# Optimization experiments

Measured on AMD Instinct MI355X. Metric: run time of the kernel, lower is better.

The kernel has to match this reference:

```python
import jax, jax.numpy as jnp
import numpy as np

B, N, K = 32, 64, 128          # batch, atoms per cell, channel width (128x0e + 128x1o)
R_MAX = 5.0
NUM_BESSEL = 8
P_CUT = 5                       # num_polynomial_cutoff
AVG_NEIGH = 16.0                # avg_num_neighbors
H_MLP = 512                     # hidden_dimensions_size, n_hidden_dimensions = 2
FEAT = 5 * K                    # ((num_interactions-1)*4 + 1) * 128 = 640


def silu(x):
    return x * jax.nn.sigmoid(x)


def _bessel_cutoff(r, mask):
    # Bessel radial basis * polynomial cutoff (MACE), masked on valid edges.
    n = jnp.arange(1, NUM_BESSEL + 1, dtype=r.dtype)
    rb = jnp.sqrt(2.0 / R_MAX) * jnp.sin(n * (jnp.pi / R_MAX) * r[..., None]) / r[..., None]
    u = r / R_MAX
    p = float(P_CUT)
    fc = 1.0 - 0.5 * (p + 1) * (p + 2) * u**P_CUT + p * (p + 2) * u**(P_CUT + 1) - 0.5 * p * (p + 1) * u**(P_CUT + 2)
    fc = fc * (u < 1.0)
    return rb * (fc * mask)[..., None]


def _sph(uvec):
    # Real spherical harmonics l=0,1,2 (component normalization), uvec: unit edge vectors.
    x, y, z = uvec[..., 0], uvec[..., 1], uvec[..., 2]
    s3, s5, s15 = 3.0**0.5, 5.0**0.5, 15.0**0.5
    Y0 = jnp.ones_like(x)[..., None]
    Y1 = jnp.stack([s3 * x, s3 * y, s3 * z], -1)
    Y2 = jnp.stack([s15 * x * y, s15 * y * z, 0.5 * s5 * (3 * z * z - 1.0),
                    s15 * x * z, 0.5 * s15 * (x * x - y * y)], -1)
    return Y0, Y1, Y2


def _radial_mlp(x, w0, b0, w1, b1, w2, b2, w3, b3):
    h = silu(x @ w0 + b0)
    h = silu(h @ w1 + b1)
    h = silu(h @ w2 + b2)
    return h @ w3 + b3


def setup_inputs() -> dict:
    key = jax.random.key(0)
    ks = jax.random.split(key, 32)
    f32 = jnp.float32

    def lin(k, fan_in, shape):
        return (jax.random.normal(k, shape, dtype=f32) / np.sqrt(fan_in)).astype(f32)

    inp = {
        "noisy_relative_positions": jax.random.uniform(ks[0], (B, N, 3), dtype=f32),
        "time": jax.random.uniform(ks[1], (B, 1), dtype=f32),
        "unit_cell": (11.0 * jnp.eye(3, dtype=f32) + 0.3 * jax.random.uniform(ks[2], (B, 3, 3), dtype=f32)),
        "w_embed": lin(ks[3], 1, (K,)),
        # interaction 1 radial MLP: 8 -> 64 -> 64 -> 64 -> 3*K (weights for l=0,1,2 paths)
        "r1_w0": lin(ks[4], NUM_BESSEL, (NUM_BESSEL, 64)), "r1_b0": jnp.zeros((64,), f32),
        "r1_w1": lin(ks[5], 64, (64, 64)), "r1_b1": jnp.zeros((64,), f32),
        "r1_w2": lin(ks[6], 64, (64, 64)), "r1_b2": jnp.zeros((64,), f32),
        "r1_w3": lin(ks[7], 64, (64, 3 * K)), "r1_b3": jnp.zeros((3 * K,), f32),
        "mix1_l0": lin(ks[8], K, (K, K)),
        "mix1_l1": lin(ks[9], K, (K, K)),
        "mix1_l2": lin(ks[10], K, (K, K)),
        # interaction 2 radial MLP: 8 -> 64 -> 64 -> 64 -> 2*K (paths 0e x 0e -> 0e, 1o x 1o -> 0e)
        "r2_w0": lin(ks[11], NUM_BESSEL, (NUM_BESSEL, 64)), "r2_b0": jnp.zeros((64,), f32),
        "r2_w1": lin(ks[12], 64, (64, 64)), "r2_b1": jnp.zeros((64,), f32),
        "r2_w2": lin(ks[13], 64, (64, 64)), "r2_b2": jnp.zeros((64,), f32),
        "r2_w3": lin(ks[14], 64, (64, 2 * K)), "r2_b3": jnp.zeros((2 * K,), f32),
        "mix2": lin(ks[15], K, (K, K)),
        # readout MLP: 641 -> 512 -> 512 -> 3
        "mlp_w0": lin(ks[16], FEAT + 1, (FEAT + 1, H_MLP)), "mlp_b0": jnp.zeros((H_MLP,), f32),
        "mlp_w1": lin(ks[17], H_MLP, (H_MLP, H_MLP)), "mlp_b1": jnp.zeros((H_MLP,), f32),
        "mlp_w2": lin(ks[18], H_MLP, (H_MLP, 3)), "mlp_b2": jnp.zeros((3,), f32),
    }
    return inp


def reference(noisy_relative_positions, time, unit_cell, w_embed,
              r1_w0, r1_b0, r1_w1, r1_b1, r1_w2, r1_b2, r1_w3, r1_b3,
              mix1_l0, mix1_l1, mix1_l2,
              r2_w0, r2_b0, r2_w1, r2_b1, r2_w2, r2_b2, r2_w3, r2_b3, mix2,
              mlp_w0, mlp_b0, mlp_w1, mlp_b1, mlp_w2, mlp_b2):
    frac = noisy_relative_positions                      # [B,N,3] fractional
    d = frac[:, :, None, :] - frac[:, None, :, :]        # [B,N,N,3]
    d = d - jnp.round(d)                                 # minimum-image PBC
    dc = jnp.einsum('bijc,bcd->bijd', d, unit_cell)      # cartesian displacements
    r = jnp.sqrt(jnp.maximum(jnp.sum(dc * dc, -1), 1e-12))
    mask = (r < R_MAX) & (~jnp.eye(N, dtype=bool))[None]
    r_safe = jnp.where(mask, r, 1.0)
    uvec = dc / r_safe[..., None] * mask[..., None]      # unit edge vectors (0 off-edge)

    rad = _bessel_cutoff(r_safe, mask)                   # [B,N,N,8]
    Y0, Y1, Y2 = _sph(uvec)                              # [B,N,N,1|3|5]

    h0 = jnp.broadcast_to(w_embed, (B, N, K))            # element embedding (single species)

    # ---- interaction 1: radial-weighted tensor product h_j (x) Y_l, scatter over j ----
    we = _radial_mlp(rad, r1_w0, r1_b0, r1_w1, r1_b1, r1_w2, r1_b2, r1_w3, r1_b3)
    we = we.reshape(B, N, N, 3, K) * mask[..., None, None]
    hj = h0[:, None, :, :]                               # sender features [B,1,N,K]
    msg0 = jnp.einsum('bijk,bijm->bimk', we[..., 0, :] * hj, Y0)[:, :, 0] / AVG_NEIGH  # [B,N,K]
    msg1 = jnp.einsum('bijk,bijm->bimk', we[..., 1, :] * hj, Y1) / AVG_NEIGH           # [B,N,3,K]
    msg2 = jnp.einsum('bijk,bijm->bimk', we[..., 2, :] * hj, Y2) / AVG_NEIGH           # [B,N,5,K]

    s1 = msg0 @ mix1_l0 + jnp.sum(msg2 * msg2, axis=2) @ mix1_l2   # scalars [B,N,K]
    v1 = jnp.einsum('bimk,kc->bimc', msg1, mix1_l1)                # vectors [B,N,3,K]
    h1 = silu(s1)

    # ---- interaction 2: scalar output from 0e x 0e and 1o x 1o -> 0e paths ----
    we2 = _radial_mlp(rad, r2_w0, r2_b0, r2_w1, r2_b1, r2_w2, r2_b2, r2_w3, r2_b3)
    we2 = we2.reshape(B, N, N, 2, K) * mask[..., None, None]
    msg_a = jnp.sum(we2[..., 0, :] * h1[:, None, :, :], axis=2)    # [B,N,K]
    inv = jnp.einsum('bijm,bjmk->bijk', Y1, v1)                    # Y1 . v1_j invariant
    msg_b = jnp.sum(we2[..., 1, :] * inv, axis=2)
    s2 = ((msg_a + msg_b) / AVG_NEIGH) @ mix2                      # [B,N,K]

    # node_feats: layer1 full irreps (128x0e + 128x1o -> 512) + layer2 scalars (128) = 640
    node_feats = jnp.concatenate([s1, v1.reshape(B, N, 3 * K), s2], axis=-1)

    t = jnp.broadcast_to(time[:, None, :], (B, N, 1))
    x = jnp.concatenate([node_feats, t], axis=-1)                  # [B,N,641]
    x = jax.nn.relu(x @ mlp_w0 + mlp_b0)
    x = jax.nn.relu(x @ mlp_w1 + mlp_b1)
    return x @ mlp_w2 + mlp_b2                                     # [B,N,3]
```

## Files before the change

kernel.cpp:

```cpp
#include <hip/hip_runtime.h>
#include <math.h>

#define B_ 32
#define N_ 64
#define K_ 128
#define NPAIR (B_*N_*N_)
#define NTRI 2080
#define GEOM_BLOCKS 260
#define PREP_COUNT 741376
#define PREP_BLOCKS 2896

typedef __attribute__((ext_vector_type(8))) short short8;
typedef __attribute__((ext_vector_type(8))) __bf16 bf16x8;
typedef __attribute__((ext_vector_type(4))) float floatx4;

__device__ __forceinline__ float silu_f(float x) {
    float e = __builtin_amdgcn_exp2f(-1.442695040888963f * x);
    return x * __builtin_amdgcn_rcpf(1.0f + e);
}
__device__ __forceinline__ float4 ld4(const float* p) { return *(const float4*)p; }

__device__ __forceinline__ short f2bf(float x) {
    union { float f; unsigned u; } v; v.f = x;
    unsigned r = (v.u + 0x7FFFu + ((v.u >> 16) & 1u)) >> 16;
    return (short)r;
}
__device__ __forceinline__ float bf2f(short s) {
    union { unsigned u; float f; } v;
    v.u = ((unsigned)(unsigned short)s) << 16;
    return v.f;
}
__device__ __forceinline__ bf16x8 ld_frag(const short* p) {
    short8 r = *(const short8*)p;
    return __builtin_bit_cast(bf16x8, r);
}

__device__ __forceinline__ int2 tri_decode(int t) {
    float f = (129.0f - sqrtf((float)(16641 - 8*t))) * 0.5f;
    int i = (int)f;
    int off = 64*i - (i*(i-1))/2;
    if (off > t) { i--; off = 64*i - (i*(i-1))/2; }
    else {
        int offn = 64*(i+1) - ((i+1)*i)/2;
        if (offn <= t) { i = i+1; off = offn; }
    }
    return make_int2(i, i + (t - off));
}

__global__ __launch_bounds__(256) void pre_kernel(
    const float* __restrict__ pos, const float* __restrict__ cell,
    short* __restrict__ radbf, float* __restrict__ Y1, float* __restrict__ Y2,
    float* __restrict__ maskf,
    const float* __restrict__ r1w0, const float* __restrict__ r1w1,
    const float* __restrict__ r1w2, const float* __restrict__ r1w3,
    const float* __restrict__ r2w0, const float* __restrict__ r2w1,
    const float* __restrict__ r2w2, const float* __restrict__ r2w3,
    const float* __restrict__ r2b3,
    const float* __restrict__ mw0, const float* __restrict__ mw1,
    const float* __restrict__ wemb,
    const float* __restrict__ l0, const float* __restrict__ l1,
    const float* __restrict__ l2, short* __restrict__ dst)
{
    int t = threadIdx.x;
    if (blockIdx.x < GEOM_BLOCKS) {
        int gt = blockIdx.x * 256 + t;
        int b = gt / NTRI;
        int tt = gt - b*NTRI;
        int2 ij = tri_decode(tt);
        int i = ij.x, j = ij.y;
        const float* pi = pos + (size_t)(b*N_ + i)*3;
        const float* pj = pos + (size_t)(b*N_ + j)*3;
        float d0 = pi[0]-pj[0], d1 = pi[1]-pj[1], d2 = pi[2]-pj[2];
        d0 -= rintf(d0); d1 -= rintf(d1); d2 -= rintf(d2);
        const float* C = cell + b*9;
        float dc0 = d0*C[0] + d1*C[3] + d2*C[6];
        float dc1 = d0*C[1] + d1*C[4] + d2*C[7];
        float dc2 = d0*C[2] + d1*C[5] + d2*C[8];
        float r2 = fmaxf(dc0*dc0 + dc1*dc1 + dc2*dc2, 1e-12f);
        float r = sqrtf(r2);
        bool m = (r < 5.0f) && (i != j);
        float mf = m ? 1.0f : 0.0f;
        float rs = m ? r : 1.0f;
        float inv_rs = __builtin_amdgcn_rcpf(rs);
        inv_rs = inv_rs * (2.0f - rs*inv_rs);
        float x = dc0*inv_rs*mf, y = dc1*inv_rs*mf, z = dc2*inv_rs*mf;
        float u = r * 0.2f;
        float u2 = u*u, u4 = u2*u2, u5 = u4*u;
        float fc = 1.0f - 21.0f*u5 + 35.0f*u5*u - 15.0f*u5*u2;
        fc = (u < 1.0f) ? fc : 0.0f;
        float pref = 0.6324555320336759f * inv_rs * (fc * mf);
        float rev = 0.1f * rs;
        float sw = __builtin_amdgcn_sinf(rev);
        float cw = __builtin_amdgcn_cosf(rev);
        float c2 = 2.0f * cw;
        short8 sv;
        float sp = 0.f, s = sw;
        #pragma unroll
        for (int n = 0; n < 8; n++) {
            sv[n] = f2bf(pref * s);
            float ns = c2*s - sp;
            sp = s; s = ns;
        }
        size_t pu = ((size_t)b*64 + i)*64 + j;
        size_t pl = ((size_t)b*64 + j)*64 + i;
        *(short8*)&radbf[pu*8] = sv;
        const float s3  = 1.7320508075688772f;
        const float s5  = 2.23606797749979f;
        const float s15 = 3.872983346207417f;
        float y1x = s3*x, y1y = s3*y, y1z = s3*z;
        Y1[pu*3+0] = y1x; Y1[pu*3+1] = y1y; Y1[pu*3+2] = y1z;
        Y1[pl*3+0] = -y1x; Y1[pl*3+1] = -y1y; Y1[pl*3+2] = -y1z;
        float q0 = s15*x*y, q1 = s15*y*z, q2 = 0.5f*s5*(3.0f*z*z - 1.0f);
        float q3 = s15*x*z, q4 = 0.5f*s15*(x*x - y*y);
        Y2[pu*5+0]=q0; Y2[pu*5+1]=q1; Y2[pu*5+2]=q2; Y2[pu*5+3]=q3; Y2[pu*5+4]=q4;
        Y2[pl*5+0]=q0; Y2[pl*5+1]=q1; Y2[pl*5+2]=q2; Y2[pl*5+3]=q3; Y2[pl*5+4]=q4;
        maskf[pu] = mf; maskf[pl] = mf;
        return;
    }
    int idx = (blockIdx.x - GEOM_BLOCKS) * 256 + t;
    if (idx >= PREP_COUNT) return;
    short v;
    if (idx < 4096) {
        int n = idx >> 6, k = idx & 63; v = f2bf(r1w1[k*64 + n]);
    } else if (idx < 8192) {
        int i = idx - 4096; int n = i >> 6, k = i & 63; v = f2bf(r1w2[k*64 + n]);
    } else if (idx < 12288) {
        int i = idx - 8192; int n = i >> 6, k = i & 63; v = f2bf(r2w1[k*64 + n]);
    } else if (idx < 16384) {
        int i = idx - 12288; int n = i >> 6, k = i & 63; v = f2bf(r2w2[k*64 + n]);
    } else if (idx < 40960) {
        int i = idx - 16384; int col = i / 96, k = i - col*96;
        v = (k < 64) ? f2bf(r2w3[k*256 + col])
          : (k == 64) ? f2bf(r2b3[col]) : (short)0;
    } else if (idx < 401408) {
        int i = idx - 40960; int n = i / 704, k = i - n*704;
        v = (k < 641) ? f2bf(mw0[(size_t)k*512 + n]) : (short)0;
    } else if (idx < 663552) {
        int i = idx - 401408; int n = i >> 9, k = i & 511;
        v = f2bf(mw1[(size_t)k*512 + n]);
    } else if (idx < 665600) {
        int i = idx - 663552; int n = i >> 5, k = i & 31;
        v = (k < 8) ? f2bf(r1w0[k*64 + n]) : (short)0;
    } else if (idx < 667648) {
        int i = idx - 665600; int n = i >> 5, k = i & 31;
        v = (k < 8) ? f2bf(r2w0[k*64 + n]) : (short)0;
    } else if (idx < 692224) {
        int i = idx - 667648; int col = i >> 6, h = i & 63;
        v = f2bf(r1w3[h*384 + col] * wemb[col & 127] * 0.0625f);
    } else {
        int i = idx - 692224; int n = i / 384, k = i - n*384;
        float f;
        if (k < 128)       f = l0[k*128 + n];
        else if (k < 256)  f = l2[(k-128)*128 + n];
        else               f = l1[(k-256)*128 + n];
        v = f2bf(f);
    }
    dst[idx] = v;
}

__global__ __launch_bounds__(256) void bigmlp_kernel(
    const short* __restrict__ radbf,
    const short* __restrict__ w0T1, const float* __restrict__ b01,
    const short* __restrict__ w1T1, const float* __restrict__ b11,
    const short* __restrict__ w2T1, const float* __restrict__ b21,
    short* __restrict__ hc1,
    const short* __restrict__ w0T2, const float* __restrict__ b02,
    const short* __restrict__ w1T2, const float* __restrict__ b12,
    const short* __restrict__ w2T2, const float* __restrict__ b22,
    short* __restrict__ hc2)
{
    __shared__ short radB[128*40];
    __shared__ short actA[128*72];
    __shared__ short actB[128*72];
    __shared__ int prs[128];
    int t = threadIdx.x;
    int wv = t >> 6, lane = t & 63, qd = lane >> 4, nn = lane & 15;
    int bb = blockIdx.x / 17;
    int chunk = blockIdx.x - bb*17;

    if (t < 128) {
        int tt0 = chunk*128 + t;
        uint4 z = {0,0,0,0};
        uint4 rv = z;
        int pr = -1;
        if (tt0 < NTRI) {
            int2 ij = tri_decode(tt0);
            pr = (ij.x << 8) | ij.y;
            size_t pu = ((size_t)bb*64 + ij.x)*64 + ij.y;
            rv = *(const uint4*)&radbf[pu*8];
        }
        prs[t] = pr;
        *(uint4*)&radB[t*40]      = rv;
        *(uint4*)&radB[t*40 + 8]  = z;
        *(uint4*)&radB[t*40 + 16] = z;
        *(uint4*)&radB[t*40 + 24] = z;
        *(uint4*)&radB[t*40 + 32] = z;
    }
    __syncthreads();

    const short* w0Ts[2] = {w0T1, w0T2};
    const short* w1Ts[2] = {w1T1, w1T2};
    const short* w2Ts[2] = {w2T1, w2T2};
    const float* b0s[2]  = {b01, b02};
    const float* b1s[2]  = {b11, b12};
    const float* b2s[2]  = {b21, b22};
    short* hcs[2] = {hc1, hc2};

    for (int net = 0; net < 2; net++) {
        const short* w0T = w0Ts[net];
        const short* w1T = w1Ts[net];
        const short* w2T = w2Ts[net];
        const float* b0 = b0s[net];
        const float* b1 = b1s[net];
        const float* b2 = b2s[net];
        short* hc = hcs[net];
        #pragma unroll
        for (int ms = 0; ms < 2; ms++) {
            int r0 = wv*32 + ms*16;
            bf16x8 a = ld_frag(&radB[(r0 + nn)*40 + qd*8]);
            #pragma unroll
            for (int tt = 0; tt < 4; tt++) {
                floatx4 acc = (floatx4){0.f,0.f,0.f,0.f};
                bf16x8 bb_ = ld_frag(&w0T[(tt*16 + nn)*32 + qd*8]);
                acc = __builtin_amdgcn_mfma_f32_16x16x32_bf16(a, bb_, acc, 0, 0, 0);
                int col = tt*16 + nn;
                float bv = b0[col];
                #pragma unroll
                for (int i = 0; i < 4; i++)
                    actA[(r0 + qd*4 + i)*72 + col] = f2bf(silu_f(acc[i] + bv));
            }
        }
        __syncthreads();
        #pragma unroll
        for (int ms = 0; ms < 2; ms++) {
            int r0 = wv*32 + ms*16;
            bf16x8 a0 = ld_frag(&actA[(r0 + nn)*72 + qd*8]);
            bf16x8 a1 = ld_frag(&actA[(r0 + nn)*72 + 32 + qd*8]);
            #pragma unroll
            for (int tt = 0; tt < 4; tt++) {
                floatx4 acc = (floatx4){0.f,0.f,0.f,0.f};
                bf16x8 b0f = ld_frag(&w1T[(tt*16 + nn)*64 + qd*8]);
                bf16x8 b1f = ld_frag(&w1T[(tt*16 + nn)*64 + 32 + qd*8]);
                acc = __builtin_amdgcn_mfma_f32_16x16x32_bf16(a0, b0f, acc, 0, 0, 0);
                acc = __builtin_amdgcn_mfma_f32_16x16x32_bf16(a1, b1f, acc, 0, 0, 0);
                int col = tt*16 + nn;
                float bv = b1[col];
                #pragma unroll
                for (int i = 0; i < 4; i++)
                    actB[(r0 + qd*4 + i)*72 + col] = f2bf(silu_f(acc[i] + bv));
            }
        }
        __syncthreads();
        #pragma unroll
        for (int ms = 0; ms < 2; ms++) {
            int r0 = wv*32 + ms*16;
            bf16x8 a0 = ld_frag(&actB[(r0 + nn)*72 + qd*8]);
            bf16x8 a1 = ld_frag(&actB[(r0 + nn)*72 + 32 + qd*8]);
            #pragma unroll
            for (int tt = 0; tt < 4; tt++) {
                floatx4 acc = (floatx4){0.f,0.f,0.f,0.f};
                bf16x8 b0f = ld_frag(&w2T[(tt*16 + nn)*64 + qd*8]);
                bf16x8 b1f = ld_frag(&w2T[(tt*16 + nn)*64 + 32 + qd*8]);
                acc = __builtin_amdgcn_mfma_f32_16x16x32_bf16(a0, b0f, acc, 0, 0, 0);
                acc = __builtin_amdgcn_mfma_f32_16x16x32_bf16(a1, b1f, acc, 0, 0, 0);
                int col = tt*16 + nn;
                float bv = b2[col];
                #pragma unroll
                for (int i = 0; i < 4; i++) {
                    int pr = prs[r0 + qd*4 + i];
                    if (pr >= 0) {
                        short val = f2bf(silu_f(acc[i] + bv));
                        int pi = pr >> 8, pj = pr & 255;
                        size_t base = (size_t)bb*4096;
                        hc[(base + pi*64 + pj)*64 + col] = val;
                        if (pi != pj)
                            hc[(base + pj*64 + pi)*64 + col] = val;
                    }
                }
            }
        }
        __syncthreads();
    }
}

__global__ __launch_bounds__(256) void msg1_kernel(
    const short* __restrict__ hc1, const float* __restrict__ Y1g,
    const float* __restrict__ Y2g, const float* __restrict__ maskg,
    const float* __restrict__ wemb, const float* __restrict__ b3,
    const short* __restrict__ w3T, const short* __restrict__ lT,
    const float* __restrict__ timeg,
    short* __restrict__ h1bf, float* __restrict__ v1g, short* __restrict__ featsb)
{
    __shared__ __align__(16) char pool[19008];
    short* hcT  = (short*)pool;
    short* A2   = (short*)pool;
    short* YmB  = (short*)(pool + 9216);
    short* GB   = (short*)(pool + 11520);
    float* msgF = (float*)(pool + 13824);
    float* qF   = (float*)(pool + 18432);
    float* SY   = (float*)(pool + 18944);

    int t = threadIdx.x;
    int wv = t >> 6, lane = t & 63, qd = lane >> 4, nn = lane & 15;
    int node = blockIdx.x;
    int b = node >> 6;
    size_t pbase = (size_t)node * 64;

    for (int idx = t; idx < 512; idx += 256) {
        int j = idx >> 3, h0 = (idx & 7)*8;
        short8 v = *(const short8*)&hc1[((size_t)node*64 + j)*64 + h0];
        #pragma unroll
        for (int q = 0; q < 8; q++) hcT[(h0 + q)*72 + j] = v[q];
    }
    for (int idx = t; idx < 1152; idx += 256) YmB[idx] = 0;
    __syncthreads();
    if (t < 64) {
        int j = t;
        float mf = maskg[pbase + j];
        YmB[j] = f2bf(mf);
        #pragma unroll
        for (int m = 0; m < 3; m++) YmB[(1+m)*72 + j] = f2bf(Y1g[(pbase+j)*3 + m] * mf);
        #pragma unroll
        for (int m = 0; m < 5; m++) YmB[(4+m)*72 + j] = f2bf(Y2g[(pbase+j)*5 + m] * mf);
    }
    __syncthreads();
    if (t < 16) {
        float acc = 0.f;
        if (t < 9) for (int j = 0; j < 64; j++) acc += bf2f(YmB[t*72 + j]);
        SY[t] = acc;
    }
    {
        floatx4 accG = (floatx4){0.f,0.f,0.f,0.f};
        #pragma unroll
        for (int ks = 0; ks < 64; ks += 32) {
            bf16x8 a = ld_frag(&YmB[nn*72 + ks + qd*8]);
            bf16x8 bfr = ld_frag(&hcT[(wv*16 + nn)*72 + ks + qd*8]);
            accG = __builtin_amdgcn_mfma_f32_16x16x32_bf16(a, bfr, accG, 0, 0, 0);
        }
        #pragma unroll
        for (int i = 0; i < 4; i++)
            GB[(qd*4 + i)*72 + wv*16 + nn] = f2bf(accG[i]);
    }
    __syncthreads();
    {
        bf16x8 a0f = ld_frag(&GB[nn*72 + 0  + qd*8]);
        bf16x8 a1f = ld_frag(&GB[nn*72 + 32 + qd*8]);
        #pragma unroll
        for (int tl = 0; tl < 6; tl++) {
            int col0 = (wv*6 + tl)*16;
            floatx4 acc = (floatx4){0.f,0.f,0.f,0.f};
            bf16x8 b0f = ld_frag(&w3T[(col0 + nn)*64 + 0  + qd*8]);
            bf16x8 b1f = ld_frag(&w3T[(col0 + nn)*64 + 32 + qd*8]);
            acc = __builtin_amdgcn_mfma_f32_16x16x32_bf16(a0f, b0f, acc, 0, 0, 0);
            acc = __builtin_amdgcn_mfma_f32_16x16x32_bf16(a1f, b1f, acc, 0, 0, 0);
            int col = col0 + nn;
            int csec = col >> 7, k = col & 127;
            #pragma unroll
            for (int i = 0; i < 4; i++) {
                int m = qd*4 + i;
                bool valid = (csec == 0) ? (m == 0)
                           : (csec == 1) ? (m >= 1 && m <= 3)
                                         : (m >= 4 && m <= 8);
                if (valid)
                    msgF[m*128 + k] = acc[i] + SY[m]*b3[col]*wemb[k]*0.0625f;
            }
        }
    }
    __syncthreads();
    if (t < 128) {
        float acc = 0.f;
        #pragma unroll
        for (int m = 4; m < 9; m++) { float v = msgF[m*128 + t]; acc += v*v; }
        qF[t] = acc;
    }
    __syncthreads();
    for (int idx = t; idx < 6272; idx += 256) A2[idx] = 0;
    __syncthreads();
    A2[t] = (t < 128) ? f2bf(msgF[t]) : f2bf(qF[t - 128]);
    if (t < 128) {
        #pragma unroll
        for (int m = 1; m <= 3; m++)
            A2[m*392 + 256 + t] = f2bf(msgF[m*128 + t]);
    }
    __syncthreads();
    #pragma unroll
    for (int tt = 0; tt < 2; tt++) {
        int col = (wv*2 + tt)*16 + nn;
        floatx4 acc = (floatx4){0.f,0.f,0.f,0.f};
        #pragma unroll
        for (int ks = 0; ks < 384; ks += 32) {
            bf16x8 a = ld_frag(&A2[nn*392 + ks + qd*8]);
            bf16x8 bfr = ld_frag(&lT[(size_t)col*384 + ks + qd*8]);
            acc = __builtin_amdgcn_mfma_f32_16x16x32_bf16(a, bfr, acc, 0, 0, 0);
        }
        if (qd == 0) {
            float s1 = acc[0];
            featsb[(size_t)node*704 + col] = f2bf(s1);
            h1bf[(size_t)node*128 + col] = f2bf(silu_f(s1));
            #pragma unroll
            for (int i = 1; i < 4; i++) {
                float v = acc[i];
                v1g[(size_t)node*384 + (i-1)*128 + col] = v;
                featsb[(size_t)node*704 + 128 + (i-1)*128 + col] = f2bf(v);
            }
        }
    }
    if (t == 0) featsb[(size_t)node*704 + 640] = f2bf(timeg[b]);
    if (t < 63) featsb[(size_t)node*704 + 641 + t] = 0;
}

__global__ __launch_bounds__(256) void msg2_kernel(
    const short* __restrict__ hc2, const float* __restrict__ Y1g,
    const float* __restrict__ maskg, const short* __restrict__ w3extT,
    const short* __restrict__ h1bf, const float* __restrict__ v1g,
    const float* __restrict__ mix2, short* __restrict__ featsb)
{
    __shared__ __align__(16) char pool[50688];
    short* hc2e  = (short*)pool;
    short* h1B   = (short*)(pool + 14336);
    short* invB  = (short*)(pool + 31744);
    float* Y1s   = (float*)(pool + 49152);
    float* msgab = (float*)(pool + 50176);

    int t = threadIdx.x;
    int wv = t >> 6, lane = t & 63, qd = lane >> 4, nn = lane & 15;
    int node = blockIdx.x;
    int b = node >> 6;
    size_t pbase = (size_t)node * 64;

    if (t < 64) {
        int j = t;
        #pragma unroll
        for (int m = 0; m < 3; m++) Y1s[j*4 + m] = Y1g[(pbase+j)*3 + m];
        float mf = maskg[pbase + j];
        short8 z8 = {0,0,0,0,0,0,0,0};
        *(short8*)&hc2e[j*112 + 64] = z8;
        *(short8*)&hc2e[j*112 + 72] = z8;
        *(short8*)&hc2e[j*112 + 80] = z8;
        *(short8*)&hc2e[j*112 + 88] = z8;
        *(short8*)&hc2e[j*112 + 96] = z8;
        *(short8*)&hc2e[j*112 + 104] = z8;
        hc2e[j*112 + 64] = f2bf(mf);
    }
    for (int idx = t; idx < 512; idx += 256) {
        int j = idx >> 3, h0 = (idx & 7)*8;
        short8 v = *(const short8*)&hc2[((size_t)node*64 + j)*64 + h0];
        float mf = maskg[pbase + j];
        if (mf == 0.f) { short8 z8 = {0,0,0,0,0,0,0,0}; v = z8; }
        *(short8*)&hc2e[j*112 + h0] = v;
    }
    for (int idx = t; idx < 1024; idx += 256) {
        int j = idx >> 4, k0 = (idx & 15)*8;
        *(uint4*)&h1B[j*136 + k0] = *(const uint4*)&h1bf[((size_t)b*64 + j)*128 + k0];
    }
    if (t < 128) msgab[t] = 0.f;
    __syncthreads();
    for (int idx = t; idx < 2048; idx += 256) {
        int j = idx >> 5, kq = (idx & 31)*4;
        const float* vb = &v1g[((size_t)b*64 + j)*384 + kq];
        float4 vx = ld4(vb), vy = ld4(vb + 128), vz = ld4(vb + 256);
        float yx = Y1s[j*4+0], yy = Y1s[j*4+1], yz = Y1s[j*4+2];
        invB[j*136 + kq + 0] = f2bf(yx*vx.x + yy*vy.x + yz*vz.x);
        invB[j*136 + kq + 1] = f2bf(yx*vx.y + yy*vy.y + yz*vz.y);
        invB[j*136 + kq + 2] = f2bf(yx*vx.z + yy*vy.z + yz*vz.z);
        invB[j*136 + kq + 3] = f2bf(yx*vx.w + yy*vy.w + yz*vz.w);
    }
    __syncthreads();
    {
        bf16x8 a0 = ld_frag(&hc2e[(wv*16 + nn)*112 + 0  + qd*8]);
        bf16x8 a1 = ld_frag(&hc2e[(wv*16 + nn)*112 + 32 + qd*8]);
        bf16x8 a2 = ld_frag(&hc2e[(wv*16 + nn)*112 + 64 + qd*8]);
        for (int g = 0; g < 4; g++) {
            #pragma unroll
            for (int tt = 0; tt < 4; tt++) {
                int col0 = g*64 + tt*16;
                floatx4 acc = (floatx4){0.f,0.f,0.f,0.f};
                bf16x8 b0f = ld_frag(&w3extT[(col0 + nn)*96 + 0  + qd*8]);
                bf16x8 b1f = ld_frag(&w3extT[(col0 + nn)*96 + 32 + qd*8]);
                bf16x8 b2f = ld_frag(&w3extT[(col0 + nn)*96 + 64 + qd*8]);
                acc = __builtin_amdgcn_mfma_f32_16x16x32_bf16(a0, b0f, acc, 0, 0, 0);
                acc = __builtin_amdgcn_mfma_f32_16x16x32_bf16(a1, b1f, acc, 0, 0, 0);
                acc = __builtin_amdgcn_mfma_f32_16x16x32_bf16(a2, b2f, acc, 0, 0, 0);
                int col = col0 + nn;
                int k = col & 127;
                const short* src = (col < 128) ? h1B : invB;
                float p = 0.f;
                #pragma unroll
                for (int i = 0; i < 4; i++) {
                    int j = wv*16 + qd*4 + i;
                    p += acc[i] * bf2f(src[j*136 + k]);
                }
                p += __shfl_xor(p, 16);
                p += __shfl_xor(p, 32);
                if (qd == 0) atomicAdd(&msgab[k], p);
            }
        }
    }
    __syncthreads();
    if (t < 128) {
        float acc = 0.f;
        for (int k = 0; k < 128; k++) acc += msgab[k] * mix2[k*128 + t];
        featsb[(size_t)node*704 + 512 + t] = f2bf(acc * 0.0625f);
    }
}

__global__ __launch_bounds__(256) void gemm_part_kernel(
    const short* __restrict__ A, int lda,
    const short* __restrict__ BT, int ldb,
    int ngran, int nsplit, float* __restrict__ Cp)
{
    int t = threadIdx.x;
    int wv = t >> 6, lane = t & 63, qd = lane >> 4, nn = lane & 15;
    int m0 = blockIdx.x * 64, n0 = blockIdx.y * 64, z = blockIdx.z;
    int g0 = (z*ngran)/nsplit, g1 = ((z+1)*ngran)/nsplit;
    floatx4 acc[4];
    #pragma unroll
    for (int tt = 0; tt < 4; tt++) acc[tt] = (floatx4){0.f,0.f,0.f,0.f};
    int row = wv*16 + nn;
    for (int g = g0; g < g1; g++) {
        int k = g*32;
        bf16x8 a = ld_frag(&A[(size_t)(m0 + row)*lda + k + qd*8]);
        #pragma unroll
        for (int tt = 0; tt < 4; tt++) {
            bf16x8 bb = ld_frag(&BT[(size_t)(n0 + tt*16 + nn)*ldb + k + qd*8]);
            acc[tt] = __builtin_amdgcn_mfma_f32_16x16x32_bf16(a, bb, acc[tt], 0, 0, 0);
        }
    }
    float* out = Cp + (size_t)z*2048*512;
    #pragma unroll
    for (int tt = 0; tt < 4; tt++) {
        int n = n0 + tt*16 + nn;
        #pragma unroll
        for (int i = 0; i < 4; i++)
            out[(size_t)(m0 + wv*16 + qd*4 + i)*512 + n] = acc[tt][i];
    }
}

__global__ __launch_bounds__(256) void combine_kernel(
    const float* __restrict__ Cp, const float* __restrict__ bias,
    short* __restrict__ out)
{
    int idx = (blockIdx.x * 256 + threadIdx.x) * 4;
    int n = idx & 511;
    float4 s = ld4(&Cp[idx]);
    #pragma unroll
    for (int z = 1; z < 4; z++) {
        float4 p = ld4(&Cp[(size_t)z*1048576 + idx]);
        s.x += p.x; s.y += p.y; s.z += p.z; s.w += p.w;
    }
    float4 bv = ld4(&bias[n]);
    short4 o;
    o.x = f2bf(fmaxf(s.x + bv.x, 0.f));
    o.y = f2bf(fmaxf(s.y + bv.y, 0.f));
    o.z = f2bf(fmaxf(s.z + bv.z, 0.f));
    o.w = f2bf(fmaxf(s.w + bv.w, 0.f));
    *(short4*)&out[idx] = o;
}

__global__ __launch_bounds__(64) void final3_kernel(
    const short* __restrict__ H, const float* __restrict__ w2,
    const float* __restrict__ b2, float* __restrict__ out)
{
    int node = blockIdx.x, lane = threadIdx.x;
    float a0 = 0.f, a1 = 0.f, a2 = 0.f;
    #pragma unroll
    for (int r = 0; r < 8; r++) {
        int k = r*64 + lane;
        float h = bf2f(H[(size_t)node*512 + k]);
        a0 += h * w2[k*3 + 0];
        a1 += h * w2[k*3 + 1];
        a2 += h * w2[k*3 + 2];
    }
    #pragma unroll
    for (int off = 32; off > 0; off >>= 1) {
        a0 += __shfl_down(a0, off);
        a1 += __shfl_down(a1, off);
        a2 += __shfl_down(a2, off);
    }
    if (lane == 0) {
        out[(size_t)node*3 + 0] = a0 + b2[0];
        out[(size_t)node*3 + 1] = a1 + b2[1];
        out[(size_t)node*3 + 2] = a2 + b2[2];
    }
}

extern "C" void kernel_launch(void* const* d_in, const int* in_sizes, int n_in,
                              void* d_out, int out_size, void* d_ws, size_t ws_size,
                              hipStream_t stream) {
    const float* pos   = (const float*)d_in[0];
    const float* timeg = (const float*)d_in[1];
    const float* cell  = (const float*)d_in[2];
    const float* wemb  = (const float*)d_in[3];
    const float* r1w0  = (const float*)d_in[4];
    const float* r1b0  = (const float*)d_in[5];
    const float* r1w1  = (const float*)d_in[6];
    const float* r1b1  = (const float*)d_in[7];
    const float* r1w2  = (const float*)d_in[8];
    const float* r1b2  = (const float*)d_in[9];
    const float* r1w3  = (const float*)d_in[10];
    const float* r1b3  = (const float*)d_in[11];
    const float* l0    = (const float*)d_in[12];
    const float* l1    = (const float*)d_in[13];
    const float* l2    = (const float*)d_in[14];
    const float* r2w0  = (const float*)d_in[15];
    const float* r2b0  = (const float*)d_in[16];
    const float* r2w1  = (const float*)d_in[17];
    const float* r2b1  = (const float*)d_in[18];
    const float* r2w2  = (const float*)d_in[19];
    const float* r2b2  = (const float*)d_in[20];
    const float* r2w3  = (const float*)d_in[21];
    const float* r2b3  = (const float*)d_in[22];
    const float* mix2  = (const float*)d_in[23];
    const float* mw0   = (const float*)d_in[24];
    const float* mb0   = (const float*)d_in[25];
    const float* mw1   = (const float*)d_in[26];
    const float* mb1   = (const float*)d_in[27];
    const float* mw2   = (const float*)d_in[28];
    const float* mb2   = (const float*)d_in[29];

    float* ws = (float*)d_ws;
    short* radbf  = (short*)ws;
    float* Y1     = ws + 524288;
    float* Y2     = ws + 917504;
    float* maskf  = ws + 1572864;
    float* v1     = ws + 1703936;
    short* featsb = (short*)(ws + 2490368);
    short* prep   = (short*)(ws + 3211264);
    short* hc1    = (short*)(ws + 3590144);
    short* hc2    = (short*)(ws + 7784448);
    short* h1bf   = (short*)(ws + 11978752);

    short* w1T_1  = prep;
    short* w2T_1  = prep + 4096;
    short* w1T_2  = prep + 8192;
    short* w2T_2  = prep + 12288;
    short* w3extT = prep + 16384;
    short* wT0    = prep + 40960;
    short* wT1    = prep + 401408;
    short* w0T_1  = prep + 663552;
    short* w0T_2  = prep + 665600;
    short* w3T_1  = prep + 667648;
    short* lT     = prep + 692224;

    float* Cp   = (float*)hc1;
    short* h0bb = radbf;
    short* h1bb = (short*)Y2;

    pre_kernel<<<GEOM_BLOCKS + PREP_BLOCKS, 256, 0, stream>>>(
        pos, cell, radbf, Y1, Y2, maskf,
        r1w0, r1w1, r1w2, r1w3, r2w0, r2w1, r2w2, r2w3, r2b3,
        mw0, mw1, wemb, l0, l1, l2, prep);
    bigmlp_kernel<<<32*17, 256, 0, stream>>>(radbf,
        w0T_1, r1b0, w1T_1, r1b1, w2T_1, r1b2, hc1,
        w0T_2, r2b0, w1T_2, r2b1, w2T_2, r2b2, hc2);
    msg1_kernel<<<B_*N_, 256, 0, stream>>>(hc1, Y1, Y2, maskf, wemb, r1b3,
        w3T_1, lT, timeg, h1bf, v1, featsb);
    msg2_kernel<<<B_*N_, 256, 0, stream>>>(hc2, Y1, maskf, w3extT, h1bf, v1,
        mix2, featsb);
    {
        dim3 g(32, 8, 4);
        gemm_part_kernel<<<g, 256, 0, stream>>>(featsb, 704, wT0, 704, 22, 4, Cp);
        combine_kernel<<<1024, 256, 0, stream>>>(Cp, mb0, h0bb);
        gemm_part_kernel<<<g, 256, 0, stream>>>(h0bb, 512, wT1, 512, 16, 4, Cp);
        combine_kernel<<<1024, 256, 0, stream>>>(Cp, mb1, h1bb);
    }
    final3_kernel<<<B_*N_, 64, 0, stream>>>(h1bb, mw2, mb2, (float*)d_out);
}
```

Baseline: 301.2 us.

## Split msg2 into two half-blocks per node and add separate mix2 kernel

The interaction-2 message kernel is split along a second grid dimension, so one block handles the h1 (scalar) path and the other the Y1·v1 invariant path. The bias is applied as bb*mask instead of through an extra K=32 MFMA slice, and the mix2 projection moves into a new small s2_kernel that sums the two partial messages. LDS per block shrinks, which should raise occupancy and double the block count. Separately, msg1 narrows its zero-fill to only the needed regions and drops two barriers. The cost is an extra kernel launch and a global round trip for the partial sums.

```diff
diff --git a/kernel.cpp b/kernel.cpp
--- a/kernel.cpp
+++ b/kernel.cpp
@@ -55,7 +55,6 @@
     const float* __restrict__ r1w2, const float* __restrict__ r1w3,
     const float* __restrict__ r2w0, const float* __restrict__ r2w1,
     const float* __restrict__ r2w2, const float* __restrict__ r2w3,
-    const float* __restrict__ r2b3,
     const float* __restrict__ mw0, const float* __restrict__ mw1,
     const float* __restrict__ wemb,
     const float* __restrict__ l0, const float* __restrict__ l1,
@@ -129,9 +128,8 @@
     } else if (idx < 16384) {
         int i = idx - 12288; int n = i >> 6, k = i & 63; v = f2bf(r2w2[k*64 + n]);
     } else if (idx < 40960) {
-        int i = idx - 16384; int col = i / 96, k = i - col*96;
-        v = (k < 64) ? f2bf(r2w3[k*256 + col])
-          : (k == 64) ? f2bf(r2b3[col]) : (short)0;
+        int i = idx - 16384;
+        v = (i < 16384) ? f2bf(r2w3[(i & 63)*256 + (i >> 6)]) : (short)0;
     } else if (idx < 401408) {
         int i = idx - 40960; int n = i / 704, k = i - n*704;
         v = (k < 641) ? f2bf(mw0[(size_t)k*512 + n]) : (short)0;
@@ -312,8 +310,7 @@
         #pragma unroll
         for (int q = 0; q < 8; q++) hcT[(h0 + q)*72 + j] = v[q];
     }
-    for (int idx = t; idx < 1152; idx += 256) YmB[idx] = 0;
-    __syncthreads();
+    for (int idx = t; idx < 504; idx += 256) YmB[648 + idx] = 0;
     if (t < 64) {
         int j = t;
         float mf = maskg[pbase + j];
@@ -343,6 +340,8 @@
     }
     __syncthreads();
     {
+        short8 z8 = {0,0,0,0,0,0,0,0};
+        for (int idx = t; idx < 720; idx += 256) *(short8*)&A2[idx*8] = z8;
         bf16x8 a0f = ld_frag(&GB[nn*72 + 0  + qd*8]);
         bf16x8 a1f = ld_frag(&GB[nn*72 + 32 + qd*8]);
         #pragma unroll
@@ -367,14 +366,14 @@
         }
     }
     __syncthreads();
+    A2[5760 + t] = 0;
+    A2[6016 + t] = 0;
     if (t < 128) {
         float acc = 0.f;
         #pragma unroll
         for (int m = 4; m < 9; m++) { float v = msgF[m*128 + t]; acc += v*v; }
         qF[t] = acc;
     }
-    __syncthreads();
-    for (int idx = t; idx < 6272; idx += 256) A2[idx] = 0;
     __syncthreads();
     A2[t] = (t < 128) ? f2bf(msgF[t]) : f2bf(qF[t - 128]);
     if (t < 128) {
@@ -409,86 +408,76 @@
     if (t < 63) featsb[(size_t)node*704 + 641 + t] = 0;
 }
 
-__global__ __launch_bounds__(256) void msg2_kernel(
+__global__ __launch_bounds__(256) void msg2h_kernel(
     const short* __restrict__ hc2, const float* __restrict__ Y1g,
-    const float* __restrict__ maskg, const short* __restrict__ w3extT,
+    const float* __restrict__ maskg, const short* __restrict__ w3T2,
+    const float* __restrict__ b3,
     const short* __restrict__ h1bf, const float* __restrict__ v1g,
-    const float* __restrict__ mix2, short* __restrict__ featsb)
-{
-    __shared__ __align__(16) char pool[50688];
+    float* __restrict__ msgpA, float* __restrict__ msgpB)
+{
+    __shared__ __align__(16) char pool[27648];
     short* hc2e  = (short*)pool;
-    short* h1B   = (short*)(pool + 14336);
-    short* invB  = (short*)(pool + 31744);
-    float* Y1s   = (float*)(pool + 49152);
-    float* msgab = (float*)(pool + 50176);
+    short* srcB  = (short*)(pool + 9216);
+    float* mask_s= (float*)(pool + 26624);
+    float* msgab = (float*)(pool + 26880);
 
     int t = threadIdx.x;
     int wv = t >> 6, lane = t & 63, qd = lane >> 4, nn = lane & 15;
     int node = blockIdx.x;
+    int half = blockIdx.y;
     int b = node >> 6;
     size_t pbase = (size_t)node * 64;
 
-    if (t < 64) {
-        int j = t;
-        #pragma unroll
-        for (int m = 0; m < 3; m++) Y1s[j*4 + m] = Y1g[(pbase+j)*3 + m];
-        float mf = maskg[pbase + j];
-        short8 z8 = {0,0,0,0,0,0,0,0};
-        *(short8*)&hc2e[j*112 + 64] = z8;
-        *(short8*)&hc2e[j*112 + 72] = z8;
-        *(short8*)&hc2e[j*112 + 80] = z8;
-        *(short8*)&hc2e[j*112 + 88] = z8;
-        *(short8*)&hc2e[j*112 + 96] = z8;
-        *(short8*)&hc2e[j*112 + 104] = z8;
-        hc2e[j*112 + 64] = f2bf(mf);
-    }
+    if (t < 64) mask_s[t] = maskg[pbase + t];
     for (int idx = t; idx < 512; idx += 256) {
         int j = idx >> 3, h0 = (idx & 7)*8;
         short8 v = *(const short8*)&hc2[((size_t)node*64 + j)*64 + h0];
         float mf = maskg[pbase + j];
         if (mf == 0.f) { short8 z8 = {0,0,0,0,0,0,0,0}; v = z8; }
-        *(short8*)&hc2e[j*112 + h0] = v;
-    }
-    for (int idx = t; idx < 1024; idx += 256) {
-        int j = idx >> 4, k0 = (idx & 15)*8;
-        *(uint4*)&h1B[j*136 + k0] = *(const uint4*)&h1bf[((size_t)b*64 + j)*128 + k0];
+        *(short8*)&hc2e[j*72 + h0] = v;
+    }
+    if (half == 0) {
+        for (int idx = t; idx < 1024; idx += 256) {
+            int j = idx >> 4, k0 = (idx & 15)*8;
+            *(uint4*)&srcB[j*136 + k0] = *(const uint4*)&h1bf[((size_t)b*64 + j)*128 + k0];
+        }
+    } else {
+        for (int idx = t; idx < 2048; idx += 256) {
+            int j = idx >> 5, kq = (idx & 31)*4;
+            const float* vb = &v1g[((size_t)b*64 + j)*384 + kq];
+            float4 vx = ld4(vb), vy = ld4(vb + 128), vz = ld4(vb + 256);
+            const float* yp = &Y1g[(pbase + j)*3];
+            float yx = yp[0], yy = yp[1], yz = yp[2];
+            srcB[j*136 + kq + 0] = f2bf(yx*vx.x + yy*vy.x + yz*vz.x);
+            srcB[j*136 + kq + 1] = f2bf(yx*vx.y + yy*vy.y + yz*vz.y);
+            srcB[j*136 + kq + 2] = f2bf(yx*vx.z + yy*vy.z + yz*vz.z);
+            srcB[j*136 + kq + 3] = f2bf(yx*vx.w + yy*vy.w + yz*vz.w);
+        }
     }
     if (t < 128) msgab[t] = 0.f;
     __syncthreads();
-    for (int idx = t; idx < 2048; idx += 256) {
-        int j = idx >> 5, kq = (idx & 31)*4;
-        const float* vb = &v1g[((size_t)b*64 + j)*384 + kq];
-        float4 vx = ld4(vb), vy = ld4(vb + 128), vz = ld4(vb + 256);
-        float yx = Y1s[j*4+0], yy = Y1s[j*4+1], yz = Y1s[j*4+2];
-        invB[j*136 + kq + 0] = f2bf(yx*vx.x + yy*vy.x + yz*vz.x);
-        invB[j*136 + kq + 1] = f2bf(yx*vx.y + yy*vy.y + yz*vz.y);
-        invB[j*136 + kq + 2] = f2bf(yx*vx.z + yy*vy.z + yz*vz.z);
-        invB[j*136 + kq + 3] = f2bf(yx*vx.w + yy*vy.w + yz*vz.w);
-    }
-    __syncthreads();
     {
-        bf16x8 a0 = ld_frag(&hc2e[(wv*16 + nn)*112 + 0  + qd*8]);
-        bf16x8 a1 = ld_frag(&hc2e[(wv*16 + nn)*112 + 32 + qd*8]);
-        bf16x8 a2 = ld_frag(&hc2e[(wv*16 + nn)*112 + 64 + qd*8]);
-        for (int g = 0; g < 4; g++) {
+        bf16x8 a0 = ld_frag(&hc2e[(wv*16 + nn)*72 + qd*8]);
+        bf16x8 a1 = ld_frag(&hc2e[(wv*16 + nn)*72 + 32 + qd*8]);
+        int gbase = half*2;
+        for (int g = gbase; g < gbase + 2; g++) {
             #pragma unroll
             for (int tt = 0; tt < 4; tt++) {
                 int col0 = g*64 + tt*16;
+                int col = col0 + nn;
                 floatx4 acc = (floatx4){0.f,0.f,0.f,0.f};
-                bf16x8 b0f = ld_frag(&w3extT[(col0 + nn)*96 + 0  + qd*8]);
-                bf16x8 b1f = ld_frag(&w3extT[(col0 + nn)*96 + 32 + qd*8]);
-                bf16x8 b2f = ld_frag(&w3extT[(col0 + nn)*96 + 64 + qd*8]);
+                bf16x8 b0f = ld_frag(&w3T2[(size_t)col*64 + qd*8]);
+                bf16x8 b1f = ld_frag(&w3T2[(size_t)col*64 + 32 + qd*8]);
                 acc = __builtin_amdgcn_mfma_f32_16x16x32_bf16(a0, b0f, acc, 0, 0, 0);
                 acc = __builtin_amdgcn_mfma_f32_16x16x32_bf16(a1, b1f, acc, 0, 0, 0);
-                acc = __builtin_amdgcn_mfma_f32_16x16x32_bf16(a2, b2f, acc, 0, 0, 0);
-                int col = col0 + nn;
                 int k = col & 127;
-                const short* src = (col < 128) ? h1B : invB;
+                float bb = b3[col];
                 float p = 0.f;
                 #pragma unroll
                 for (int i = 0; i < 4; i++) {
                     int j = wv*16 + qd*4 + i;
-                    p += acc[i] * bf2f(src[j*136 + k]);
+                    float we = acc[i] + bb*mask_s[j];
+                    p += we * bf2f(srcB[j*136 + k]);
                 }
                 p += __shfl_xor(p, 16);
                 p += __shfl_xor(p, 32);
@@ -498,10 +487,23 @@
     }
     __syncthreads();
     if (t < 128) {
-        float acc = 0.f;
-        for (int k = 0; k < 128; k++) acc += msgab[k] * mix2[k*128 + t];
-        featsb[(size_t)node*704 + 512 + t] = f2bf(acc * 0.0625f);
-    }
+        float* dst = (half == 0) ? msgpA : msgpB;
+        dst[(size_t)node*128 + t] = msgab[t];
+    }
+}
+
+__global__ __launch_bounds__(128) void s2_kernel(
+    const float* __restrict__ msgpA, const float* __restrict__ msgpB,
+    const float* __restrict__ mix2, short* __restrict__ featsb)
+{
+    __shared__ float s[128];
+    int t = threadIdx.x;
+    int node = blockIdx.x;
+    s[t] = msgpA[(size_t)node*128 + t] + msgpB[(size_t)node*128 + t];
+    __syncthreads();
+    float acc = 0.f;
+    for (int k = 0; k < 128; k++) acc += s[k] * mix2[k*128 + t];
+    featsb[(size_t)node*704 + 512 + t] = f2bf(acc * 0.0625f);
 }
 
 __global__ __launch_bounds__(256) void gemm_part_kernel(
@@ -634,7 +636,7 @@
     short* w2T_1  = prep + 4096;
     short* w1T_2  = prep + 8192;
     short* w2T_2  = prep + 12288;
-    short* w3extT = prep + 16384;
+    short* w3T2   = prep + 16384;
     short* wT0    = prep + 40960;
     short* wT1    = prep + 401408;
     short* w0T_1  = prep + 663552;
@@ -642,21 +644,27 @@
     short* w3T_1  = prep + 667648;
     short* lT     = prep + 692224;
 
-    float* Cp   = (float*)hc1;
-    short* h0bb = radbf;
-    short* h1bb = (short*)Y2;
+    float* msgpA = ws;
+    float* msgpB = ws + 262144;
+    float* Cp    = (float*)hc1;
+    short* h0bb  = radbf;
+    short* h1bb  = (short*)Y2;
 
     pre_kernel<<<GEOM_BLOCKS + PREP_BLOCKS, 256, 0, stream>>>(
         pos, cell, radbf, Y1, Y2, maskf,
-        r1w0, r1w1, r1w2, r1w3, r2w0, r2w1, r2w2, r2w3, r2b3,
+        r1w0, r1w1, r1w2, r1w3, r2w0, r2w1, r2w2, r2w3,
         mw0, mw1, wemb, l0, l1, l2, prep);
     bigmlp_kernel<<<32*17, 256, 0, stream>>>(radbf,
         w0T_1, r1b0, w1T_1, r1b1, w2T_1, r1b2, hc1,
         w0T_2, r2b0, w1T_2, r2b1, w2T_2, r2b2, hc2);
     msg1_kernel<<<B_*N_, 256, 0, stream>>>(hc1, Y1, Y2, maskf, wemb, r1b3,
         w3T_1, lT, timeg, h1bf, v1, featsb);
-    msg2_kernel<<<B_*N_, 256, 0, stream>>>(hc2, Y1, maskf, w3extT, h1bf, v1,
-        mix2, featsb);
+    {
+        dim3 g(B_*N_, 2);
+        msg2h_kernel<<<g, 256, 0, stream>>>(hc2, Y1, maskf, w3T2, r2b3,
+            h1bf, v1, msgpA, msgpB);
+    }
+    s2_kernel<<<B_*N_, 128, 0, stream>>>(msgpA, msgpB, mix2, featsb);
     {
         dim3 g(32, 8, 4);
         gemm_part_kernel<<<g, 256, 0, stream>>>(featsb, 704, wT0, 704, 22, 4, Cp);
```

After: 306.3 us. No clear change (+1.7%).
